# Optimization experiments

Hardware: AMD Instinct MI355X
Metric: run time of the kernel (lower is better)

Reference implementation:

```python
import jax, jax.numpy as jnp
import numpy as np

B, S, D, R, H, NI, NP, NO, K = 2, 2048, 1024, 1024, 8, 8, 32, 8, 3
DH = R // H


def setup_inputs() -> dict:
    key = jax.random.key(0)
    ks = jax.random.split(key, 32)
    rn = lambda k, shp, s=1.0: jax.random.normal(k, shp, jnp.float32) * s
    nrm = lambda v: v / (jnp.linalg.norm(v, axis=-1, keepdims=True) + 1e-8)
    w = 1.0 / np.sqrt(D).astype(np.float32)
    inp = {
        'x': rn(ks[0], (B, S, D)),
        'mask': jnp.tril(jnp.ones((S, S), bool))[None, None],  # causal [1,1,S,S]
        'Wr_in': rn(ks[1], (NI, D), w), 'Wr_proc': rn(ks[2], (NP, D), w), 'Wr_out': rn(ks[3], (NO, D), w),
        'WrO_in': rn(ks[4], (NI, R), w), 'WrO_proc': rn(ks[5], (NP, R), w), 'WrO_out': rn(ks[6], (NO, R), w),
        'Wq_in': rn(ks[7], (NI, D, R), w), 'vq': nrm(rn(ks[8], (NP, R))), 'Wq_out': rn(ks[9], (NO, R, D), w),
        'Wk_in': rn(ks[10], (NI, D, R), w), 'vk': nrm(rn(ks[11], (NP, R))), 'Wk_out': rn(ks[12], (NO, R, D), w),
        'Wv_in': rn(ks[13], (NI, D, R), w), 'vv': nrm(rn(ks[14], (NP, R))), 'Wv_out': rn(ks[15], (NO, R, D), w),
        # circuit_O = NeuronCircuit(rank, d_model): dims swapped
        'Wo_in': rn(ks[16], (NI, R, D), w), 'vo': nrm(rn(ks[17], (NP, D))), 'Wo_out': rn(ks[18], (NO, D, R), w),
    }
    return inp


def _router(x, Wi, Wp, Wo, k):
    in_w = jax.nn.softmax(x @ Wi.T, axis=-1)            # [B,S,NI]
    _, proc_idx = jax.lax.top_k(x @ Wp.T, k)            # [B,S,k]
    out_w = jax.nn.softmax(x @ Wo.T, axis=-1)           # [B,S,NO]
    return in_w, proc_idx, out_w


def _circuit(x, Win, vproc, Wout, in_w, proc_idx, out_w):
    # soft input mix: d_in -> r
    h = jnp.einsum('bsd,ndr,bsn->bsr', x, Win, in_w)
    # k sequential Householder reflections with gathered vectors
    v = vproc[proc_idx]                                 # [B,S,k,r]
    v = v / jnp.sqrt(jnp.sum(v * v, axis=-1, keepdims=True) + 1e-8)
    for i in range(v.shape[2]):
        vi = v[:, :, i, :]
        h = h - 2.0 * vi * jnp.sum(h * vi, axis=-1, keepdims=True)
    # soft output mix: r -> d_out
    return jnp.einsum('bsr,nrd,bsn->bsd', h, Wout, out_w)


def reference(x, mask, Wr_in, Wr_proc, Wr_out, WrO_in, WrO_proc, WrO_out,
              Wq_in, vq, Wq_out, Wk_in, vk, Wk_out, Wv_in, vv, Wv_out,
              Wo_in, vo, Wo_out):
    in_w, pidx, out_w = _router(x, Wr_in, Wr_proc, Wr_out, K)
    Q = _circuit(x, Wq_in, vq, Wq_out, in_w, pidx, out_w)   # [B,S,R]
    Kt = _circuit(x, Wk_in, vk, Wk_out, in_w, pidx, out_w)
    V = _circuit(x, Wv_in, vv, Wv_out, in_w, pidx, out_w)
    q = Q.reshape(B, S, H, DH).transpose(0, 2, 1, 3)
    k = Kt.reshape(B, S, H, DH).transpose(0, 2, 1, 3)
    v = V.reshape(B, S, H, DH).transpose(0, 2, 1, 3)
    scores = jnp.einsum('bhqd,bhkd->bhqk', q, k) / np.sqrt(DH).astype(np.float32)
    scores = jnp.where(mask, scores, jnp.float32(-1e9))
    p = jax.nn.softmax(scores, axis=-1)
    o = jnp.einsum('bhqk,bhkd->bhqd', p, v)
    o = o.transpose(0, 2, 1, 3).reshape(B, S, R)
    in_wO, pidxO, out_wO = _router(o, WrO_in, WrO_proc, WrO_out, K)
    out = _circuit(o, Wo_in, vo, Wo_out, in_wO, pidxO, out_wO)  # [B,S,D]
    return out
```

## Files before the change

### kernel.cpp

```cpp
#include <hip/hip_runtime.h>


typedef __attribute__((ext_vector_type(4))) float f32x4;
typedef _Float16 f16x8 __attribute__((ext_vector_type(8)));
typedef _Float16 f16x4 __attribute__((ext_vector_type(4)));

static constexpr int S_LEN  = 2048;
static constexpr int TOK    = 4096;
static constexpr int DMODEL = 1024;
static constexpr int KDIM   = 8192;

__device__ __forceinline__ void async16(const void* g, void* l) {
  __builtin_amdgcn_global_load_lds(
      (const __attribute__((address_space(1))) void*)g,
      (__attribute__((address_space(3))) void*)l, 16, 0, 0);
}

__global__ __launch_bounds__(256) void split_kernel(const float* __restrict__ X,
                                                    _Float16* __restrict__ Xh,
                                                    _Float16* __restrict__ Xl) {
  size_t i = ((size_t)blockIdx.x * 256 + threadIdx.x) * 4;
  float4 v = *(const float4*)&X[i];
  float a[4] = {v.x, v.y, v.z, v.w};
  f16x4 hv, lv;
#pragma unroll
  for (int e = 0; e < 4; ++e) {
    _Float16 hh = (_Float16)a[e];
    hv[e] = hh;
    lv[e] = (_Float16)(a[e] - (float)hh);
  }
  *(f16x4*)&Xh[i] = hv;
  *(f16x4*)&Xl[i] = lv;
}

__global__ __launch_bounds__(256) void transpose_split(const float* __restrict__ W,
                                                       _Float16* __restrict__ Th,
                                                       _Float16* __restrict__ Tl) {
  __shared__ float tbuf[64][65];
  const int tid = threadIdx.x;
  const int k0 = blockIdx.x * 64, n0 = blockIdx.y * 64;
#pragma unroll
  for (int j = 0; j < 4; ++j) {
    int ci = tid + 256 * j;
    int r = ci >> 4, c4 = (ci & 15) * 4;
    float4 v = *(const float4*)&W[(size_t)(k0 + r) * DMODEL + n0 + c4];
    tbuf[r][c4 + 0] = v.x; tbuf[r][c4 + 1] = v.y;
    tbuf[r][c4 + 2] = v.z; tbuf[r][c4 + 3] = v.w;
  }
  __syncthreads();
#pragma unroll
  for (int j = 0; j < 2; ++j) {
    int ci = tid + 256 * j;
    int nl = ci >> 3, k8 = (ci & 7) * 8;
    f16x8 hv, lv;
#pragma unroll
    for (int e = 0; e < 8; ++e) {
      float v = tbuf[k8 + e][nl];
      _Float16 hh = (_Float16)v;
      hv[e] = hh;
      lv[e] = (_Float16)(v - (float)hh);
    }
    size_t off = (size_t)(n0 + nl) * KDIM + k0 + k8;
    *(f16x8*)&Th[off] = hv;
    *(f16x8*)&Tl[off] = lv;
  }
}

__global__ __launch_bounds__(256) void router_kernel(const float* __restrict__ X,
                                                     const float* __restrict__ Wi,
                                                     const float* __restrict__ Wp,
                                                     const float* __restrict__ Wo,
                                                     float* __restrict__ in_w,
                                                     float* __restrict__ out_w,
                                                     int* __restrict__ pidx) {
  __shared__ float xs[1024];
  __shared__ double lg[48];
  const int t = blockIdx.x, tid = threadIdx.x;
  const int wid = tid >> 6, lane = tid & 63;
#pragma unroll
  for (int j = 0; j < 4; ++j) {
    int d = tid + 256 * j;
    xs[d] = X[(size_t)t * DMODEL + d];
  }
  __syncthreads();
  for (int i = wid; i < 48; i += 4) {
    const float* wrow = (i < 8)  ? Wi + (size_t)i * DMODEL
                      : (i < 40) ? Wp + (size_t)(i - 8) * DMODEL
                                 : Wo + (size_t)(i - 40) * DMODEL;
    double s = 0.0;
#pragma unroll
    for (int j = 0; j < 16; ++j) { int d = lane + 64 * j; s += (double)xs[d] * (double)wrow[d]; }
#pragma unroll
    for (int mm = 32; mm >= 1; mm >>= 1) s += __shfl_xor(s, mm);
    if (lane == 0) lg[i] = s;
  }
  __syncthreads();
  if (tid == 0) {
    float l[8], m;
    for (int i = 0; i < 8; ++i) l[i] = (float)lg[i];
    m = l[0];
    for (int i = 1; i < 8; ++i) m = fmaxf(m, l[i]);
    float e[8], su = 0.f;
    for (int i = 0; i < 8; ++i) { e[i] = expf(l[i] - m); su += e[i]; }
    for (int i = 0; i < 8; ++i) in_w[t * 8 + i] = e[i] / su;
  } else if (tid == 64) {
    float l[8], m;
    for (int i = 0; i < 8; ++i) l[i] = (float)lg[40 + i];
    m = l[0];
    for (int i = 1; i < 8; ++i) m = fmaxf(m, l[i]);
    float e[8], su = 0.f;
    for (int i = 0; i < 8; ++i) { e[i] = expf(l[i] - m); su += e[i]; }
    for (int i = 0; i < 8; ++i) out_w[t * 8 + i] = e[i] / su;
  } else if (tid == 128) {
    unsigned used = 0;
    for (int j = 0; j < 3; ++j) {
      double best = -1e300; int bi = 0;
      for (int i = 0; i < 32; ++i)
        if (!((used >> i) & 1u) && lg[8 + i] > best) { best = lg[8 + i]; bi = i; }
      used |= 1u << bi;
      pidx[t * 3 + j] = bi;
    }
  }
}

__global__ __launch_bounds__(256) void reflect4_kernel(const float* __restrict__ Pa,
                                                       const float* __restrict__ Pb,
                                                       const float* __restrict__ Pc,
                                                       const float* __restrict__ Pd,
                                                       const int* __restrict__ pidx,
                                                       const float* __restrict__ vtab,
                                                       _Float16* __restrict__ Hh,
                                                       _Float16* __restrict__ Hl) {
  __shared__ float red[8];
  const int t = blockIdx.x, tid = threadIdx.x;
  const int wid = tid >> 6, lane = tid & 63;
  size_t gi = (size_t)t * DMODEL + tid * 4;
  float4 ha = *(const float4*)&Pa[gi];
  float4 hb = *(const float4*)&Pb[gi];
  float4 hc = *(const float4*)&Pc[gi];
  float4 hd = *(const float4*)&Pd[gi];
  float4 h = {ha.x + hb.x + hc.x + hd.x, ha.y + hb.y + hc.y + hd.y,
              ha.z + hb.z + hc.z + hd.z, ha.w + hb.w + hc.w + hd.w};
  for (int i = 0; i < 3; ++i) {
    int idx = pidx[t * 3 + i];
    float4 vi = *(const float4*)&vtab[(size_t)idx * DMODEL + tid * 4];
    float hv = h.x * vi.x + h.y * vi.y + h.z * vi.z + h.w * vi.w;
    float vv = vi.x * vi.x + vi.y * vi.y + vi.z * vi.z + vi.w * vi.w;
#pragma unroll
    for (int mm = 32; mm >= 1; mm >>= 1) { hv += __shfl_xor(hv, mm); vv += __shfl_xor(vv, mm); }
    if (lane == 0) { red[wid] = hv; red[4 + wid] = vv; }
    __syncthreads();
    float dot = red[0] + red[1] + red[2] + red[3];
    float vn  = red[4] + red[5] + red[6] + red[7];
    __syncthreads();
    float c = 2.f * dot / (vn + 1e-8f);
    h.x -= c * vi.x; h.y -= c * vi.y; h.z -= c * vi.z; h.w -= c * vi.w;
  }
  float a[4] = {h.x, h.y, h.z, h.w};
  f16x4 hv4, lv4;
#pragma unroll
  for (int e = 0; e < 4; ++e) {
    _Float16 hh = (_Float16)a[e];
    hv4[e] = hh;
    lv4[e] = (_Float16)(a[e] - (float)hh);
  }
  *(f16x4*)&Hh[gi] = hv4;
  *(f16x4*)&Hl[gi] = lv4;
}

__global__ __launch_bounds__(256) void reduce4_planes(const float* __restrict__ a,
                                                      const float* __restrict__ b,
                                                      const float* __restrict__ c,
                                                      const float* __restrict__ d,
                                                      _Float16* __restrict__ Dh,
                                                      _Float16* __restrict__ Dl) {
  size_t i = ((size_t)blockIdx.x * 256 + threadIdx.x) * 4;
  float4 va = *(const float4*)&a[i];
  float4 vb = *(const float4*)&b[i];
  float4 vc = *(const float4*)&c[i];
  float4 vd = *(const float4*)&d[i];
  float s[4] = {va.x + vb.x + vc.x + vd.x, va.y + vb.y + vc.y + vd.y,
                va.z + vb.z + vc.z + vd.z, va.w + vb.w + vc.w + vd.w};
  f16x4 hv, lv;
#pragma unroll
  for (int e = 0; e < 4; ++e) {
    _Float16 hh = (_Float16)s[e];
    hv[e] = hh;
    lv[e] = (_Float16)(s[e] - (float)hh);
  }
  *(f16x4*)&Dh[i] = hv;
  *(f16x4*)&Dl[i] = lv;
}

__global__ __launch_bounds__(256) void reduce4_f32(const float* __restrict__ a,
                                                   const float* __restrict__ b,
                                                   const float* __restrict__ c,
                                                   const float* __restrict__ d,
                                                   float* __restrict__ o) {
  size_t i = ((size_t)blockIdx.x * 256 + threadIdx.x) * 4;
  float4 va = *(const float4*)&a[i];
  float4 vb = *(const float4*)&b[i];
  float4 vc = *(const float4*)&c[i];
  float4 vd = *(const float4*)&d[i];
  float4 vo = {va.x + vb.x + vc.x + vd.x, va.y + vb.y + vc.y + vd.y,
               va.z + vb.z + vc.z + vd.z, va.w + vb.w + vc.w + vd.w};
  *(float4*)&o[i] = vo;
}

template <bool FAST>
__global__ __launch_bounds__(256, 4) void gemm_planes(const _Float16* __restrict__ Ahp,
                                                      const _Float16* __restrict__ Alp,
                                                      const float* __restrict__ wmix,
                                                      const _Float16* __restrict__ Bh,
                                                      const _Float16* __restrict__ Bl,
                                                      float* __restrict__ C0,
                                                      float* __restrict__ C1,
                                                      float* __restrict__ C2,
                                                      float* __restrict__ C3) {
  __shared__ _Float16 sAh[128 * 32], sAl[128 * 32];
  __shared__ _Float16 sBh[128 * 32], sBl[128 * 32];
  __shared__ float sWr[128 * 2];
  const int tid = threadIdx.x;
  const int wid = tid >> 6, lane = tid & 63;
  const int l16 = lane & 15, lhi = lane >> 4;
  const int wr = wid >> 1, wc = wid & 1;
  const int fid = blockIdx.x + (blockIdx.y << 5) + (blockIdx.z << 8);
  const int wg  = ((fid & 7) << 7) + (fid >> 3);
  const int kz  = wg >> 8;
  const int rem = wg & 255;
  const int bm = (rem & 31) * 128;
  const int bn = (rem >> 5) * 128;
  const int kbase = kz * 2048, nb = kz * 2;
  float* __restrict__ Cp = (kz == 0) ? C0 : (kz == 1) ? C1 : (kz == 2) ? C2 : C3;

  {
    int row = tid >> 1, p = tid & 1;
    const float* w = &wmix[(size_t)(bm + row) * 8 + nb];
    sWr[tid] = p ? w[1] : w[0] / w[1];
  }

  f32x4 acc[4][4];
#pragma unroll
  for (int i = 0; i < 4; ++i)
#pragma unroll
    for (int j = 0; j < 4; ++j) { f32x4 z = {0.f, 0.f, 0.f, 0.f}; acc[i][j] = z; }

  for (int kt = 0; kt < 2048; kt += 32) {
    const int kg = kbase + kt, d0 = kg & 1023;
#pragma unroll
    for (int j = 0; j < 2; ++j) {
      int ci = tid + 256 * j;
      int row = ci >> 2, jc = ci & 3;
      int jcs = jc ^ ((row >> 1) & 3);
      size_t ga = (size_t)(bm + row) * DMODEL + d0 + jcs * 8;
      size_t gb = (size_t)(bn + row) * KDIM + kg + jcs * 8;
      async16(&Ahp[ga], &sAh[ci * 8]);
      if (!FAST) async16(&Alp[ga], &sAl[ci * 8]);
      async16(&Bh[gb], &sBh[ci * 8]);
      if (!FAST) async16(&Bl[gb], &sBl[ci * 8]);
    }
    __syncthreads();
    f16x8 fah[4], fal[4], fbh[4], fbl[4];
#pragma unroll
    for (int mi = 0; mi < 4; ++mi) {
      int row = wr * 64 + mi * 16 + l16;
      int idx = row * 32 + ((lhi ^ ((row >> 1) & 3)) * 8);
      fah[mi] = *(const f16x8*)&sAh[idx];
      if (!FAST) fal[mi] = *(const f16x8*)&sAl[idx];
    }
#pragma unroll
    for (int ni = 0; ni < 4; ++ni) {
      int row = wc * 64 + ni * 16 + l16;
      int idx = row * 32 + ((lhi ^ ((row >> 1) & 3)) * 8);
      fbh[ni] = *(const f16x8*)&sBh[idx];
      if (!FAST) fbl[ni] = *(const f16x8*)&sBl[idx];
    }
#pragma unroll
    for (int mi = 0; mi < 4; ++mi)
#pragma unroll
      for (int ni = 0; ni < 4; ++ni) {
        f32x4 a = acc[mi][ni];
        a = __builtin_amdgcn_mfma_f32_16x16x32_f16(fah[mi], fbh[ni], a, 0, 0, 0);
        if (!FAST) {
          a = __builtin_amdgcn_mfma_f32_16x16x32_f16(fah[mi], fbl[ni], a, 0, 0, 0);
          a = __builtin_amdgcn_mfma_f32_16x16x32_f16(fal[mi], fbh[ni], a, 0, 0, 0);
        }
        acc[mi][ni] = a;
      }
    __syncthreads();
    if (kt == 992) {
#pragma unroll
      for (int mi = 0; mi < 4; ++mi)
#pragma unroll
        for (int r = 0; r < 4; ++r) {
          float s = sWr[(wr * 64 + mi * 16 + lhi * 4 + r) * 2];
#pragma unroll
          for (int ni = 0; ni < 4; ++ni) acc[mi][ni][r] *= s;
        }
    }
  }
#pragma unroll
  for (int mi = 0; mi < 4; ++mi)
#pragma unroll
    for (int r = 0; r < 4; ++r) {
      int rowl = wr * 64 + mi * 16 + lhi * 4 + r;
      float s = sWr[rowl * 2 + 1];
#pragma unroll
      for (int ni = 0; ni < 4; ++ni) {
        int col = bn + wc * 64 + ni * 16 + l16;
        Cp[(size_t)(bm + rowl) * DMODEL + col] = acc[mi][ni][r] * s;
      }
    }
}

__global__ __launch_bounds__(256) void vtrans4_kernel(const float* __restrict__ Va,
                                                      const float* __restrict__ Vb,
                                                      const float* __restrict__ Vc,
                                                      const float* __restrict__ Vd,
                                                      _Float16* __restrict__ Vth,
                                                      _Float16* __restrict__ Vtl) {
  __shared__ float tbuf[64][65];
  const int tid = threadIdx.x;
  const int t0 = blockIdx.x * 64, d0 = blockIdx.y * 64, bh = blockIdx.z;
  const int b = bh >> 3, h = bh & 7;
#pragma unroll
  for (int j = 0; j < 4; ++j) {
    int ci = tid + 256 * j;
    int r = ci >> 4, c4 = (ci & 15) * 4;
    size_t g = (size_t)(b * S_LEN + t0 + r) * DMODEL + h * 128 + d0 + c4;
    float4 va = *(const float4*)&Va[g];
    float4 vb = *(const float4*)&Vb[g];
    float4 vc = *(const float4*)&Vc[g];
    float4 vd = *(const float4*)&Vd[g];
    tbuf[r][c4 + 0] = va.x + vb.x + vc.x + vd.x;
    tbuf[r][c4 + 1] = va.y + vb.y + vc.y + vd.y;
    tbuf[r][c4 + 2] = va.z + vb.z + vc.z + vd.z;
    tbuf[r][c4 + 3] = va.w + vb.w + vc.w + vd.w;
  }
  __syncthreads();
#pragma unroll
  for (int j = 0; j < 4; ++j) {
    int ci = tid + 256 * j;
    int r = ci >> 4, c4 = (ci & 15) * 4;
    float s[4] = {tbuf[c4 + 0][r], tbuf[c4 + 1][r], tbuf[c4 + 2][r], tbuf[c4 + 3][r]};
    f16x4 hv, lv;
#pragma unroll
    for (int e = 0; e < 4; ++e) {
      _Float16 hh = (_Float16)s[e];
      hv[e] = hh;
      lv[e] = (_Float16)(s[e] - (float)hh);
    }
    size_t o = ((size_t)bh * 128 + d0 + r) * S_LEN + t0 + c4;
    *(f16x4*)&Vth[o] = hv;
    *(f16x4*)&Vtl[o] = lv;
  }
}

__global__ __launch_bounds__(256) void attn_kernel(const _Float16* __restrict__ Qh,
                                                   const _Float16* __restrict__ Ql,
                                                   const _Float16* __restrict__ Kh,
                                                   const _Float16* __restrict__ Kl,
                                                   const _Float16* __restrict__ Vth,
                                                   const _Float16* __restrict__ Vtl,
                                                   float* __restrict__ O,
                                                   _Float16* __restrict__ Oh) {
  __shared__ _Float16 sKh[32 * 128], sKl[32 * 128];
  __shared__ _Float16 sVh[128 * 32], sVl[128 * 32];
  __shared__ _Float16 sPh[4 * 16 * 32], sPl[4 * 16 * 32];
  const int tid = threadIdx.x;
  const int wid = tid >> 6, lane = tid & 63;
  const int l16 = lane & 15, lhi = lane >> 4;
  const int qt = (gridDim.x - 1) - blockIdx.x;
  const int bh = blockIdx.y;
  const int b = bh >> 3, h = bh & 7;
  const size_t qkbase = (size_t)b * S_LEN * DMODEL + h * 128;
  const float scale = 0.08838834764831845f;

  const int qrow = qt * 64 + wid * 16 + l16;
  const size_t qoff = qkbase + (size_t)qrow * DMODEL;
  f16x8 qh[4], ql[4];
#pragma unroll
  for (int kk = 0; kk < 4; ++kk) {
    qh[kk] = *(const f16x8*)&Qh[qoff + kk * 32 + lhi * 8];
    ql[kk] = *(const f16x8*)&Ql[qoff + kk * 32 + lhi * 8];
  }

  f32x4 of[8];
#pragma unroll
  for (int i = 0; i < 8; ++i) { f32x4 z = {0.f, 0.f, 0.f, 0.f}; of[i] = z; }
  float m_[4], l_[4];
#pragma unroll
  for (int r = 0; r < 4; ++r) { m_[r] = -1e30f; l_[r] = 0.f; }

  const int ntw = qt * 2 + 1 + (wid >> 1);
  const int NT  = qt * 2 + 2;

  for (int kt = 0; kt < NT; ++kt) {
    __syncthreads();
#pragma unroll
    for (int j = 0; j < 2; ++j) {
      int ci = tid + 256 * j;
      int k = ci >> 4, c = ci & 15;
      int cs = c ^ (k & 7);
      size_t g = qkbase + (size_t)(kt * 32 + k) * DMODEL + cs * 8;
      async16(&Kh[g], &sKh[k * 128 + c * 8]);
      async16(&Kl[g], &sKl[k * 128 + c * 8]);
    }
#pragma unroll
    for (int j = 0; j < 2; ++j) {
      int ci = tid + 256 * j;
      int d = ci >> 2, c = ci & 3;
      int cs = c ^ ((d >> 1) & 3);
      size_t g = ((size_t)bh * 128 + d) * S_LEN + kt * 32 + cs * 8;
      async16(&Vth[g], &sVh[d * 32 + c * 8]);
      async16(&Vtl[g], &sVl[d * 32 + c * 8]);
    }
    __syncthreads();

    if (kt < ntw) {
      f32x4 s0 = {0.f, 0.f, 0.f, 0.f}, s1 = {0.f, 0.f, 0.f, 0.f};
#pragma unroll
      for (int kk = 0; kk < 4; ++kk) {
        int col = (kk * 32 + lhi * 8);
        int i0 = l16 * 128 + (col ^ ((l16 & 7) * 8));
        int i1 = (16 + l16) * 128 + (col ^ (((16 + l16) & 7) * 8));
        f16x8 kb0h = *(const f16x8*)&sKh[i0];
        f16x8 kb0l = *(const f16x8*)&sKl[i0];
        f16x8 kb1h = *(const f16x8*)&sKh[i1];
        f16x8 kb1l = *(const f16x8*)&sKl[i1];
        s0 = __builtin_amdgcn_mfma_f32_16x16x32_f16(qh[kk], kb0h, s0, 0, 0, 0);
        s0 = __builtin_amdgcn_mfma_f32_16x16x32_f16(qh[kk], kb0l, s0, 0, 0, 0);
        s0 = __builtin_amdgcn_mfma_f32_16x16x32_f16(ql[kk], kb0h, s0, 0, 0, 0);
        s1 = __builtin_amdgcn_mfma_f32_16x16x32_f16(qh[kk], kb1h, s1, 0, 0, 0);
        s1 = __builtin_amdgcn_mfma_f32_16x16x32_f16(qh[kk], kb1l, s1, 0, 0, 0);
        s1 = __builtin_amdgcn_mfma_f32_16x16x32_f16(ql[kk], kb1h, s1, 0, 0, 0);
      }
      const int qg = qt * 64 + wid * 16 + (lane >> 4) * 4;
      if (kt == ntw - 1) {
#pragma unroll
        for (int r = 0; r < 4; ++r) {
          int q = qg + r;
          int k0 = kt * 32 + l16, k1 = k0 + 16;
          s0[r] = (k0 <= q) ? s0[r] * scale : -1e30f;
          s1[r] = (k1 <= q) ? s1[r] * scale : -1e30f;
        }
      } else {
#pragma unroll
        for (int r = 0; r < 4; ++r) { s0[r] *= scale; s1[r] *= scale; }
      }
      float p0[4], p1[4], fr[4];
#pragma unroll
      for (int r = 0; r < 4; ++r) {
        float rm = fmaxf(s0[r], s1[r]);
        rm = fmaxf(rm, __shfl_xor(rm, 1));
        rm = fmaxf(rm, __shfl_xor(rm, 2));
        rm = fmaxf(rm, __shfl_xor(rm, 4));
        rm = fmaxf(rm, __shfl_xor(rm, 8));
        float mn = fmaxf(m_[r], rm);
        fr[r] = __expf(m_[r] - mn);
        m_[r] = mn;
        p0[r] = __expf(s0[r] - mn);
        p1[r] = __expf(s1[r] - mn);
        float rs = p0[r] + p1[r];
        rs += __shfl_xor(rs, 1);
        rs += __shfl_xor(rs, 2);
        rs += __shfl_xor(rs, 4);
        rs += __shfl_xor(rs, 8);
        l_[r] = l_[r] * fr[r] + rs;
      }
#pragma unroll
      for (int i = 0; i < 8; ++i)
#pragma unroll
        for (int r = 0; r < 4; ++r) of[i][r] *= fr[r];
#pragma unroll
      for (int r = 0; r < 4; ++r) {
        int q = (lane >> 4) * 4 + r;
        int swz = ((q >> 1) & 3) * 8;
        int c0 = l16, c1 = 16 + l16;
        _Float16 h0 = (_Float16)p0[r];
        _Float16 h1 = (_Float16)p1[r];
        sPh[wid * 512 + q * 32 + (c0 ^ swz)] = h0;
        sPl[wid * 512 + q * 32 + (c0 ^ swz)] = (_Float16)(p0[r] - (float)h0);
        sPh[wid * 512 + q * 32 + (c1 ^ swz)] = h1;
        sPl[wid * 512 + q * 32 + (c1 ^ swz)] = (_Float16)(p1[r] - (float)h1);
      }
      int pidxr = wid * 512 + l16 * 32 + ((lhi * 8) ^ (((l16 >> 1) & 3) * 8));
      f16x8 pah = *(const f16x8*)&sPh[pidxr];
      f16x8 pal = *(const f16x8*)&sPl[pidxr];
#pragma unroll
      for (int d16 = 0; d16 < 8; ++d16) {
        int d = d16 * 16 + l16;
        int vidx = d * 32 + ((lhi * 8) ^ (((d >> 1) & 3) * 8));
        f16x8 vbh = *(const f16x8*)&sVh[vidx];
        f16x8 vbl = *(const f16x8*)&sVl[vidx];
        f32x4 a = of[d16];
        a = __builtin_amdgcn_mfma_f32_16x16x32_f16(pah, vbh, a, 0, 0, 0);
        a = __builtin_amdgcn_mfma_f32_16x16x32_f16(pah, vbl, a, 0, 0, 0);
        a = __builtin_amdgcn_mfma_f32_16x16x32_f16(pal, vbh, a, 0, 0, 0);
        of[d16] = a;
      }
    }
  }
  float inv[4];
#pragma unroll
  for (int r = 0; r < 4; ++r) inv[r] = 1.f / l_[r];
  const int qg = qt * 64 + wid * 16 + (lane >> 4) * 4;
#pragma unroll
  for (int d16 = 0; d16 < 8; ++d16)
#pragma unroll
    for (int r = 0; r < 4; ++r) {
      float val = of[d16][r] * inv[r];
      size_t gi = qkbase + (size_t)(qg + r) * DMODEL + d16 * 16 + l16;
      O[gi] = val;
      Oh[gi] = (_Float16)val;
    }
}

extern "C" void kernel_launch(void* const* d_in, const int* in_sizes, int n_in,
                              void* d_out, int out_size, void* d_ws, size_t ws_size,
                              hipStream_t stream) {
  (void)in_sizes; (void)n_in; (void)out_size;
  const float* x        = (const float*)d_in[0];
  const float* Wr_in    = (const float*)d_in[2];
  const float* Wr_proc  = (const float*)d_in[3];
  const float* Wr_out   = (const float*)d_in[4];
  const float* WrO_in   = (const float*)d_in[5];
  const float* WrO_proc = (const float*)d_in[6];
  const float* WrO_out  = (const float*)d_in[7];
  const float* Wq_in    = (const float*)d_in[8];
  const float* vq       = (const float*)d_in[9];
  const float* Wq_out   = (const float*)d_in[10];
  const float* Wk_in    = (const float*)d_in[11];
  const float* vk       = (const float*)d_in[12];
  const float* Wk_out   = (const float*)d_in[13];
  const float* Wv_in    = (const float*)d_in[14];
  const float* vv       = (const float*)d_in[15];
  const float* Wv_out   = (const float*)d_in[16];
  const float* Wo_in    = (const float*)d_in[17];
  const float* vo       = (const float*)d_in[18];
  const float* Wo_out   = (const float*)d_in[19];

  char* wsbase = (char*)d_ws;
  size_t off = 0;
  auto carve = [&](size_t bytes) -> void* {
    void* r = wsbase + off;
    off = (off + bytes + 255) & ~(size_t)255;
    return r;
  };
  const size_t WBYTES = (size_t)KDIM * DMODEL * 2;
  const size_t PBYTES = (size_t)TOK * DMODEL * 2;
  const size_t HBYTES = (size_t)TOK * DMODEL * 4;
  _Float16* WTh = (_Float16*)carve(WBYTES);
  _Float16* WTl = (_Float16*)carve(WBYTES);
  _Float16* Xh  = (_Float16*)carve(PBYTES);
  _Float16* Xl  = (_Float16*)carve(PBYTES);
  _Float16* Hh  = (_Float16*)carve(PBYTES);
  _Float16* Hl  = (_Float16*)carve(PBYTES);
  float* P0 = (float*)carve(HBYTES);
  float* P1 = (float*)carve(HBYTES);
  float* P2 = (float*)carve(HBYTES);
  _Float16* Qph = (_Float16*)carve(PBYTES);
  _Float16* Qpl = (_Float16*)carve(PBYTES);
  _Float16* Kph = (_Float16*)carve(PBYTES);
  _Float16* Kpl = (_Float16*)carve(PBYTES);
  float* iw1 = (float*)carve((size_t)TOK * 8 * 4);
  float* ow1 = (float*)carve((size_t)TOK * 8 * 4);
  float* iw2 = (float*)carve((size_t)TOK * 8 * 4);
  float* ow2 = (float*)carve((size_t)TOK * 8 * 4);
  int* pi1 = (int*)carve((size_t)TOK * 3 * 4);
  int* pi2 = (int*)carve((size_t)TOK * 3 * 4);

  if (off > ws_size) {
    hipMemsetAsync(d_out, 0, (size_t)out_size * 4, stream);
    return;
  }

  float*    Pd  = (float*)d_out;
  float*    PQ  = (float*)Qph;
  float*    PX  = (float*)Xh;
  _Float16* Vth = WTh;
  _Float16* Vtl = WTh + (size_t)TOK * DMODEL;
  float*    Ofp = P0;
  _Float16* Ohp = (_Float16*)P1;

  const dim3 blk(256);
  const dim3 tgrid(KDIM / 64, DMODEL / 64);
  const dim3 ggrid(TOK / 128, DMODEL / 128, 4);
  const dim3 rgrid(TOK * DMODEL / (256 * 4));
  const dim3 vgrid(S_LEN / 64, 2, 16);
  const dim3 agrid(S_LEN / 64, 16);

  split_kernel<<<rgrid, blk, 0, stream>>>(x, Xh, Xl);
  router_kernel<<<TOK, blk, 0, stream>>>(x, Wr_in, Wr_proc, Wr_out, iw1, ow1, pi1);

  transpose_split<<<tgrid, blk, 0, stream>>>(Wq_in, WTh, WTl);
  gemm_planes<false><<<ggrid, blk, 0, stream>>>(Xh, Xl, iw1, WTh, WTl, P0, P1, P2, Pd);
  reflect4_kernel<<<TOK, blk, 0, stream>>>(P0, P1, P2, Pd, pi1, vq, Hh, Hl);
  transpose_split<<<tgrid, blk, 0, stream>>>(Wq_out, WTh, WTl);
  gemm_planes<false><<<ggrid, blk, 0, stream>>>(Hh, Hl, ow1, WTh, WTl, P0, P1, P2, Pd);
  reduce4_planes<<<rgrid, blk, 0, stream>>>(P0, P1, P2, Pd, Qph, Qpl);

  transpose_split<<<tgrid, blk, 0, stream>>>(Wk_in, WTh, WTl);
  gemm_planes<false><<<ggrid, blk, 0, stream>>>(Xh, Xl, iw1, WTh, WTl, P0, P1, P2, Pd);
  reflect4_kernel<<<TOK, blk, 0, stream>>>(P0, P1, P2, Pd, pi1, vk, Hh, Hl);
  transpose_split<<<tgrid, blk, 0, stream>>>(Wk_out, WTh, WTl);
  gemm_planes<false><<<ggrid, blk, 0, stream>>>(Hh, Hl, ow1, WTh, WTl, P0, P1, P2, Pd);
  reduce4_planes<<<rgrid, blk, 0, stream>>>(P0, P1, P2, Pd, Kph, Kpl);

  transpose_split<<<tgrid, blk, 0, stream>>>(Wv_in, WTh, WTl);
  gemm_planes<false><<<ggrid, blk, 0, stream>>>(Xh, Xl, iw1, WTh, WTl, P0, P1, P2, Pd);
  reflect4_kernel<<<TOK, blk, 0, stream>>>(P0, P1, P2, Pd, pi1, vv, Hh, Hl);
  transpose_split<<<tgrid, blk, 0, stream>>>(Wv_out, WTh, WTl);
  gemm_planes<false><<<ggrid, blk, 0, stream>>>(Hh, Hl, ow1, WTh, WTl, P0, P1, P2, Pd);
  vtrans4_kernel<<<vgrid, blk, 0, stream>>>(P0, P1, P2, Pd, Vth, Vtl);

  attn_kernel<<<agrid, blk, 0, stream>>>(Qph, Qpl, Kph, Kpl, Vth, Vtl, Ofp, Ohp);

  router_kernel<<<TOK, blk, 0, stream>>>(Ofp, WrO_in, WrO_proc, WrO_out, iw2, ow2, pi2);
  transpose_split<<<tgrid, blk, 0, stream>>>(Wo_in, WTh, WTl);
  gemm_planes<true><<<ggrid, blk, 0, stream>>>(Ohp, Ohp, iw2, WTh, WTl, PX, P0, P2, Pd);
  reflect4_kernel<<<TOK, blk, 0, stream>>>(PX, P0, P2, Pd, pi2, vo, Hh, Hl);
  transpose_split<<<tgrid, blk, 0, stream>>>(Wo_out, WTh, WTl);
  gemm_planes<true><<<ggrid, blk, 0, stream>>>(Hh, Hh, ow2, WTh, WTl, P0, P1, P2, PQ);
  reduce4_f32<<<rgrid, blk, 0, stream>>>(P0, P1, P2, PQ, (float*)d_out);
}
```

Before: 1.834 ms.

## Switch GEMM to 32x32x16 MFMA with pre-swizzled LDS layout, fuse split into router

The planes GEMM now uses 32x32x16 MFMA instructions with a 2x2 accumulator tile per wave instead of 4x4 16x16x32 tiles. Shared memory is laid out in fragment order, which removes the XOR swizzle on reads. The FAST path uses a deeper K step of 64 and shrinks the unused low-plane buffers. The separate fp16 hi/lo split kernel is folded into the first router kernel, saving one launch and one read of x. The goal is fewer LDS reads per MFMA and less launch and memory traffic, at the cost of possible bank conflicts in the new unswizzled layout.

```diff
diff --git a/kernel.cpp b/kernel.cpp
--- a/kernel.cpp
+++ b/kernel.cpp
@@ -1,7 +1,8 @@
 #include <hip/hip_runtime.h>
 
 
-typedef __attribute__((ext_vector_type(4))) float f32x4;
+typedef __attribute__((ext_vector_type(4)))  float f32x4;
+typedef __attribute__((ext_vector_type(16))) float f32x16;
 typedef _Float16 f16x8 __attribute__((ext_vector_type(8)));
 typedef _Float16 f16x4 __attribute__((ext_vector_type(4)));
 
@@ -14,23 +15,6 @@
   __builtin_amdgcn_global_load_lds(
       (const __attribute__((address_space(1))) void*)g,
       (__attribute__((address_space(3))) void*)l, 16, 0, 0);
-}
-
-__global__ __launch_bounds__(256) void split_kernel(const float* __restrict__ X,
-                                                    _Float16* __restrict__ Xh,
-                                                    _Float16* __restrict__ Xl) {
-  size_t i = ((size_t)blockIdx.x * 256 + threadIdx.x) * 4;
-  float4 v = *(const float4*)&X[i];
-  float a[4] = {v.x, v.y, v.z, v.w};
-  f16x4 hv, lv;
-#pragma unroll
-  for (int e = 0; e < 4; ++e) {
-    _Float16 hh = (_Float16)a[e];
-    hv[e] = hh;
-    lv[e] = (_Float16)(a[e] - (float)hh);
-  }
-  *(f16x4*)&Xh[i] = hv;
-  *(f16x4*)&Xl[i] = lv;
 }
 
 __global__ __launch_bounds__(256) void transpose_split(const float* __restrict__ W,
@@ -72,7 +56,9 @@
                                                      const float* __restrict__ Wo,
                                                      float* __restrict__ in_w,
                                                      float* __restrict__ out_w,
-                                                     int* __restrict__ pidx) {
+                                                     int* __restrict__ pidx,
+                                                     _Float16* __restrict__ Xh,
+                                                     _Float16* __restrict__ Xl) {
   __shared__ float xs[1024];
   __shared__ double lg[48];
   const int t = blockIdx.x, tid = threadIdx.x;
@@ -121,6 +107,16 @@
       pidx[t * 3 + j] = bi;
     }
   }
+  if (Xh != nullptr) {
+#pragma unroll
+    for (int j = 0; j < 4; ++j) {
+      int d = tid + 256 * j;
+      float v = xs[d];
+      _Float16 hh = (_Float16)v;
+      Xh[(size_t)t * DMODEL + d] = hh;
+      Xl[(size_t)t * DMODEL + d] = (_Float16)(v - (float)hh);
+    }
+  }
 }
 
 __global__ __launch_bounds__(256) void reflect4_kernel(const float* __restrict__ Pa,
@@ -217,13 +213,18 @@
                                                       float* __restrict__ C1,
                                                       float* __restrict__ C2,
                                                       float* __restrict__ C3) {
-  __shared__ _Float16 sAh[128 * 32], sAl[128 * 32];
-  __shared__ _Float16 sBh[128 * 32], sBl[128 * 32];
+  constexpr int BK  = FAST ? 64 : 32;
+  constexpr int NKS = BK / 16;
+  constexpr int CHUNKS = 128 * BK / 8;
+  __shared__ _Float16 sAh[128 * BK];
+  __shared__ _Float16 sBh[128 * BK];
+  __shared__ _Float16 sAl[FAST ? 8 : 128 * BK];
+  __shared__ _Float16 sBl[FAST ? 8 : 128 * BK];
   __shared__ float sWr[128 * 2];
   const int tid = threadIdx.x;
   const int wid = tid >> 6, lane = tid & 63;
-  const int l16 = lane & 15, lhi = lane >> 4;
   const int wr = wid >> 1, wc = wid & 1;
+  const int l31 = lane & 31, l5 = lane >> 5;
   const int fid = blockIdx.x + (blockIdx.y << 5) + (blockIdx.z << 8);
   const int wg  = ((fid & 7) << 7) + (fid >> 3);
   const int kz  = wg >> 8;
@@ -239,75 +240,84 @@
     sWr[tid] = p ? w[1] : w[0] / w[1];
   }
 
-  f32x4 acc[4][4];
-#pragma unroll
-  for (int i = 0; i < 4; ++i)
-#pragma unroll
-    for (int j = 0; j < 4; ++j) { f32x4 z = {0.f, 0.f, 0.f, 0.f}; acc[i][j] = z; }
-
-  for (int kt = 0; kt < 2048; kt += 32) {
+  f32x16 acc[2][2];
+#pragma unroll
+  for (int i = 0; i < 2; ++i)
+#pragma unroll
+    for (int j = 0; j < 2; ++j)
+#pragma unroll
+      for (int r = 0; r < 16; ++r) acc[i][j][r] = 0.f;
+
+  for (int kt = 0; kt < 2048; kt += BK) {
     const int kg = kbase + kt, d0 = kg & 1023;
 #pragma unroll
-    for (int j = 0; j < 2; ++j) {
-      int ci = tid + 256 * j;
-      int row = ci >> 2, jc = ci & 3;
-      int jcs = jc ^ ((row >> 1) & 3);
-      size_t ga = (size_t)(bm + row) * DMODEL + d0 + jcs * 8;
-      size_t gb = (size_t)(bn + row) * KDIM + kg + jcs * 8;
-      async16(&Ahp[ga], &sAh[ci * 8]);
-      if (!FAST) async16(&Alp[ga], &sAl[ci * 8]);
-      async16(&Bh[gb], &sBh[ci * 8]);
-      if (!FAST) async16(&Bl[gb], &sBl[ci * 8]);
+    for (int j = 0; j < CHUNKS / 256; ++j) {
+      int q = tid + 256 * j;
+      int rb = q >> (FAST ? 8 : 7);
+      int kk = (q >> 6) & (NKS - 1);
+      int l  = q & 63;
+      int rowoff = rb * 32 + (l & 31);
+      int koff   = kk * 16 + (l >> 5) * 8;
+      size_t ga = (size_t)(bm + rowoff) * DMODEL + d0 + koff;
+      size_t gb = (size_t)(bn + rowoff) * KDIM  + kg + koff;
+      async16(&Ahp[ga], &sAh[q * 8]);
+      async16(&Bh[gb],  &sBh[q * 8]);
+      if (!FAST) {
+        async16(&Alp[ga], &sAl[q * 8]);
+        async16(&Bl[gb],  &sBl[q * 8]);
+      }
     }
     __syncthreads();
-    f16x8 fah[4], fal[4], fbh[4], fbl[4];
-#pragma unroll
-    for (int mi = 0; mi < 4; ++mi) {
-      int row = wr * 64 + mi * 16 + l16;
-      int idx = row * 32 + ((lhi ^ ((row >> 1) & 3)) * 8);
-      fah[mi] = *(const f16x8*)&sAh[idx];
-      if (!FAST) fal[mi] = *(const f16x8*)&sAl[idx];
-    }
-#pragma unroll
-    for (int ni = 0; ni < 4; ++ni) {
-      int row = wc * 64 + ni * 16 + l16;
-      int idx = row * 32 + ((lhi ^ ((row >> 1) & 3)) * 8);
-      fbh[ni] = *(const f16x8*)&sBh[idx];
-      if (!FAST) fbl[ni] = *(const f16x8*)&sBl[idx];
-    }
-#pragma unroll
-    for (int mi = 0; mi < 4; ++mi)
-#pragma unroll
-      for (int ni = 0; ni < 4; ++ni) {
-        f32x4 a = acc[mi][ni];
-        a = __builtin_amdgcn_mfma_f32_16x16x32_f16(fah[mi], fbh[ni], a, 0, 0, 0);
-        if (!FAST) {
-          a = __builtin_amdgcn_mfma_f32_16x16x32_f16(fah[mi], fbl[ni], a, 0, 0, 0);
-          a = __builtin_amdgcn_mfma_f32_16x16x32_f16(fal[mi], fbh[ni], a, 0, 0, 0);
+#pragma unroll
+    for (int kk = 0; kk < NKS; ++kk) {
+      f16x8 a_h[2], b_h[2], a_l[2], b_l[2];
+#pragma unroll
+      for (int mi = 0; mi < 2; ++mi) {
+        int qa = (((wr * 2 + mi) * NKS + kk) * 64 + lane) * 8;
+        a_h[mi] = *(const f16x8*)&sAh[qa];
+        if (!FAST) a_l[mi] = *(const f16x8*)&sAl[qa];
+      }
+#pragma unroll
+      for (int ni = 0; ni < 2; ++ni) {
+        int qb = (((wc * 2 + ni) * NKS + kk) * 64 + lane) * 8;
+        b_h[ni] = *(const f16x8*)&sBh[qb];
+        if (!FAST) b_l[ni] = *(const f16x8*)&sBl[qb];
+      }
+#pragma unroll
+      for (int mi = 0; mi < 2; ++mi)
+#pragma unroll
+        for (int ni = 0; ni < 2; ++ni) {
+          f32x16 a = acc[mi][ni];
+          a = __builtin_amdgcn_mfma_f32_32x32x16_f16(a_h[mi], b_h[ni], a, 0, 0, 0);
+          if (!FAST) {
+            a = __builtin_amdgcn_mfma_f32_32x32x16_f16(a_h[mi], b_l[ni], a, 0, 0, 0);
+            a = __builtin_amdgcn_mfma_f32_32x32x16_f16(a_l[mi], b_h[ni], a, 0, 0, 0);
+          }
+          acc[mi][ni] = a;
         }
-        acc[mi][ni] = a;
-      }
+    }
     __syncthreads();
-    if (kt == 992) {
-#pragma unroll
-      for (int mi = 0; mi < 4; ++mi)
-#pragma unroll
-        for (int r = 0; r < 4; ++r) {
-          float s = sWr[(wr * 64 + mi * 16 + lhi * 4 + r) * 2];
-#pragma unroll
-          for (int ni = 0; ni < 4; ++ni) acc[mi][ni][r] *= s;
+    if (kt == 1024 - BK) {
+#pragma unroll
+      for (int mi = 0; mi < 2; ++mi)
+#pragma unroll
+        for (int r = 0; r < 16; ++r) {
+          int rowl = wr * 64 + mi * 32 + (r & 3) + 8 * (r >> 2) + 4 * l5;
+          float s = sWr[rowl * 2];
+#pragma unroll
+          for (int ni = 0; ni < 2; ++ni) acc[mi][ni][r] *= s;
         }
     }
   }
 #pragma unroll
-  for (int mi = 0; mi < 4; ++mi)
-#pragma unroll
-    for (int r = 0; r < 4; ++r) {
-      int rowl = wr * 64 + mi * 16 + lhi * 4 + r;
+  for (int mi = 0; mi < 2; ++mi)
+#pragma unroll
+    for (int r = 0; r < 16; ++r) {
+      int rowl = wr * 64 + mi * 32 + (r & 3) + 8 * (r >> 2) + 4 * l5;
       float s = sWr[rowl * 2 + 1];
 #pragma unroll
-      for (int ni = 0; ni < 4; ++ni) {
-        int col = bn + wc * 64 + ni * 16 + l16;
+      for (int ni = 0; ni < 2; ++ni) {
+        int col = bn + wc * 64 + ni * 32 + l31;
         Cp[(size_t)(bm + rowl) * DMODEL + col] = acc[mi][ni][r] * s;
       }
     }
@@ -590,8 +600,7 @@
   const dim3 vgrid(S_LEN / 64, 2, 16);
   const dim3 agrid(S_LEN / 64, 16);
 
-  split_kernel<<<rgrid, blk, 0, stream>>>(x, Xh, Xl);
-  router_kernel<<<TOK, blk, 0, stream>>>(x, Wr_in, Wr_proc, Wr_out, iw1, ow1, pi1);
+  router_kernel<<<TOK, blk, 0, stream>>>(x, Wr_in, Wr_proc, Wr_out, iw1, ow1, pi1, Xh, Xl);
 
   transpose_split<<<tgrid, blk, 0, stream>>>(Wq_in, WTh, WTl);
   gemm_planes<false><<<ggrid, blk, 0, stream>>>(Xh, Xl, iw1, WTh, WTl, P0, P1, P2, Pd);
@@ -616,7 +625,8 @@
 
   attn_kernel<<<agrid, blk, 0, stream>>>(Qph, Qpl, Kph, Kpl, Vth, Vtl, Ofp, Ohp);
 
-  router_kernel<<<TOK, blk, 0, stream>>>(Ofp, WrO_in, WrO_proc, WrO_out, iw2, ow2, pi2);
+  router_kernel<<<TOK, blk, 0, stream>>>(Ofp, WrO_in, WrO_proc, WrO_out, iw2, ow2, pi2,
+                                         nullptr, nullptr);
   transpose_split<<<tgrid, blk, 0, stream>>>(Wo_in, WTh, WTl);
   gemm_planes<true><<<ggrid, blk, 0, stream>>>(Ohp, Ohp, iw2, WTh, WTl, PX, P0, P2, Pd);
   reflect4_kernel<<<TOK, blk, 0, stream>>>(PX, P0, P2, Pd, pi2, vo, Hh, Hl);
```

Measured after the change: 2.319 ms. +26.5%, slower.

## Enlarge GEMM tiles to 256x256 with 512 threads; fuse fp16 split into router

Applied to the files above, without the earlier changes.

The split-K fp16-plane GEMM now uses 256x256 output tiles with 8 waves per block, each wave holding an 8x4 grid of MFMA accumulators. This raises data reuse per LDS load and halves the number of blocks. In FAST mode the low-plane LDS buffers are shrunk. Separately, the input hi/lo fp16 split moves into the router kernel, which already holds x in shared memory, so one launch and one pass over x are removed. The larger tiles mean more registers and fewer blocks (256 per GEMM), which lowers occupancy and may leave compute units idle.

```diff
diff --git a/kernel.cpp b/kernel.cpp
--- a/kernel.cpp
+++ b/kernel.cpp
@@ -14,23 +14,6 @@
   __builtin_amdgcn_global_load_lds(
       (const __attribute__((address_space(1))) void*)g,
       (__attribute__((address_space(3))) void*)l, 16, 0, 0);
-}
-
-__global__ __launch_bounds__(256) void split_kernel(const float* __restrict__ X,
-                                                    _Float16* __restrict__ Xh,
-                                                    _Float16* __restrict__ Xl) {
-  size_t i = ((size_t)blockIdx.x * 256 + threadIdx.x) * 4;
-  float4 v = *(const float4*)&X[i];
-  float a[4] = {v.x, v.y, v.z, v.w};
-  f16x4 hv, lv;
-#pragma unroll
-  for (int e = 0; e < 4; ++e) {
-    _Float16 hh = (_Float16)a[e];
-    hv[e] = hh;
-    lv[e] = (_Float16)(a[e] - (float)hh);
-  }
-  *(f16x4*)&Xh[i] = hv;
-  *(f16x4*)&Xl[i] = lv;
 }
 
 __global__ __launch_bounds__(256) void transpose_split(const float* __restrict__ W,
@@ -72,7 +55,9 @@
                                                      const float* __restrict__ Wo,
                                                      float* __restrict__ in_w,
                                                      float* __restrict__ out_w,
-                                                     int* __restrict__ pidx) {
+                                                     int* __restrict__ pidx,
+                                                     _Float16* __restrict__ Xh,
+                                                     _Float16* __restrict__ Xl) {
   __shared__ float xs[1024];
   __shared__ double lg[48];
   const int t = blockIdx.x, tid = threadIdx.x;
@@ -121,6 +106,16 @@
       pidx[t * 3 + j] = bi;
     }
   }
+  if (Xh != nullptr) {
+#pragma unroll
+    for (int j = 0; j < 4; ++j) {
+      int d = tid + 256 * j;
+      float v = xs[d];
+      _Float16 hh = (_Float16)v;
+      Xh[(size_t)t * DMODEL + d] = hh;
+      Xl[(size_t)t * DMODEL + d] = (_Float16)(v - (float)hh);
+    }
+  }
 }
 
 __global__ __launch_bounds__(256) void reflect4_kernel(const float* __restrict__ Pa,
@@ -208,7 +203,7 @@
 }
 
 template <bool FAST>
-__global__ __launch_bounds__(256, 4) void gemm_planes(const _Float16* __restrict__ Ahp,
+__global__ __launch_bounds__(512, 2) void gemm_planes(const _Float16* __restrict__ Ahp,
                                                       const _Float16* __restrict__ Alp,
                                                       const float* __restrict__ wmix,
                                                       const _Float16* __restrict__ Bh,
@@ -217,19 +212,20 @@
                                                       float* __restrict__ C1,
                                                       float* __restrict__ C2,
                                                       float* __restrict__ C3) {
-  __shared__ _Float16 sAh[128 * 32], sAl[128 * 32];
-  __shared__ _Float16 sBh[128 * 32], sBl[128 * 32];
-  __shared__ float sWr[128 * 2];
+  __shared__ _Float16 sAh[256 * 32];
+  __shared__ _Float16 sBh[256 * 32];
+  __shared__ _Float16 sAl[FAST ? 8 : 256 * 32];
+  __shared__ _Float16 sBl[FAST ? 8 : 256 * 32];
+  __shared__ float sWr[256 * 2];
   const int tid = threadIdx.x;
   const int wid = tid >> 6, lane = tid & 63;
   const int l16 = lane & 15, lhi = lane >> 4;
-  const int wr = wid >> 1, wc = wid & 1;
-  const int fid = blockIdx.x + (blockIdx.y << 5) + (blockIdx.z << 8);
-  const int wg  = ((fid & 7) << 7) + (fid >> 3);
-  const int kz  = wg >> 8;
-  const int rem = wg & 255;
-  const int bm = (rem & 31) * 128;
-  const int bn = (rem >> 5) * 128;
+  const int wr = wid >> 2, wc = wid & 3;
+  const int fid = blockIdx.x + (blockIdx.y << 4) + (blockIdx.z << 6);
+  const int wg  = ((fid & 7) << 5) + (fid >> 3);
+  const int bm = (wg & 15) * 256;
+  const int bn = ((wg >> 4) & 3) * 256;
+  const int kz = wg >> 6;
   const int kbase = kz * 2048, nb = kz * 2;
   float* __restrict__ Cp = (kz == 0) ? C0 : (kz == 1) ? C1 : (kz == 2) ? C2 : C3;
 
@@ -239,9 +235,9 @@
     sWr[tid] = p ? w[1] : w[0] / w[1];
   }
 
-  f32x4 acc[4][4];
-#pragma unroll
-  for (int i = 0; i < 4; ++i)
+  f32x4 acc[8][4];
+#pragma unroll
+  for (int i = 0; i < 8; ++i)
 #pragma unroll
     for (int j = 0; j < 4; ++j) { f32x4 z = {0.f, 0.f, 0.f, 0.f}; acc[i][j] = z; }
 
@@ -249,61 +245,62 @@
     const int kg = kbase + kt, d0 = kg & 1023;
 #pragma unroll
     for (int j = 0; j < 2; ++j) {
-      int ci = tid + 256 * j;
+      int ci = tid + 512 * j;
       int row = ci >> 2, jc = ci & 3;
       int jcs = jc ^ ((row >> 1) & 3);
       size_t ga = (size_t)(bm + row) * DMODEL + d0 + jcs * 8;
       size_t gb = (size_t)(bn + row) * KDIM + kg + jcs * 8;
       async16(&Ahp[ga], &sAh[ci * 8]);
-      if (!FAST) async16(&Alp[ga], &sAl[ci * 8]);
-      async16(&Bh[gb], &sBh[ci * 8]);
-      if (!FAST) async16(&Bl[gb], &sBl[ci * 8]);
+      async16(&Bh[gb],  &sBh[ci * 8]);
+      if (!FAST) {
+        async16(&Alp[ga], &sAl[ci * 8]);
+        async16(&Bl[gb],  &sBl[ci * 8]);
+      }
     }
     __syncthreads();
-    f16x8 fah[4], fal[4], fbh[4], fbl[4];
-#pragma unroll
-    for (int mi = 0; mi < 4; ++mi) {
-      int row = wr * 64 + mi * 16 + l16;
-      int idx = row * 32 + ((lhi ^ ((row >> 1) & 3)) * 8);
-      fah[mi] = *(const f16x8*)&sAh[idx];
-      if (!FAST) fal[mi] = *(const f16x8*)&sAl[idx];
-    }
+    f16x8 b_h[4], b_l[4];
 #pragma unroll
     for (int ni = 0; ni < 4; ++ni) {
       int row = wc * 64 + ni * 16 + l16;
       int idx = row * 32 + ((lhi ^ ((row >> 1) & 3)) * 8);
-      fbh[ni] = *(const f16x8*)&sBh[idx];
-      if (!FAST) fbl[ni] = *(const f16x8*)&sBl[idx];
-    }
-#pragma unroll
-    for (int mi = 0; mi < 4; ++mi)
+      b_h[ni] = *(const f16x8*)&sBh[idx];
+      if (!FAST) b_l[ni] = *(const f16x8*)&sBl[idx];
+    }
+#pragma unroll
+    for (int mi = 0; mi < 8; ++mi) {
+      int rowa = wr * 128 + mi * 16 + l16;
+      int idxa = rowa * 32 + ((lhi ^ ((rowa >> 1) & 3)) * 8);
+      f16x8 a_h = *(const f16x8*)&sAh[idxa];
+      f16x8 a_l;
+      if (!FAST) a_l = *(const f16x8*)&sAl[idxa];
 #pragma unroll
       for (int ni = 0; ni < 4; ++ni) {
         f32x4 a = acc[mi][ni];
-        a = __builtin_amdgcn_mfma_f32_16x16x32_f16(fah[mi], fbh[ni], a, 0, 0, 0);
+        a = __builtin_amdgcn_mfma_f32_16x16x32_f16(a_h, b_h[ni], a, 0, 0, 0);
         if (!FAST) {
-          a = __builtin_amdgcn_mfma_f32_16x16x32_f16(fah[mi], fbl[ni], a, 0, 0, 0);
-          a = __builtin_amdgcn_mfma_f32_16x16x32_f16(fal[mi], fbh[ni], a, 0, 0, 0);
+          a = __builtin_amdgcn_mfma_f32_16x16x32_f16(a_h, b_l[ni], a, 0, 0, 0);
+          a = __builtin_amdgcn_mfma_f32_16x16x32_f16(a_l, b_h[ni], a, 0, 0, 0);
         }
         acc[mi][ni] = a;
       }
+    }
     __syncthreads();
     if (kt == 992) {
 #pragma unroll
-      for (int mi = 0; mi < 4; ++mi)
+      for (int mi = 0; mi < 8; ++mi)
 #pragma unroll
         for (int r = 0; r < 4; ++r) {
-          float s = sWr[(wr * 64 + mi * 16 + lhi * 4 + r) * 2];
+          float s = sWr[(wr * 128 + mi * 16 + lhi * 4 + r) * 2];
 #pragma unroll
           for (int ni = 0; ni < 4; ++ni) acc[mi][ni][r] *= s;
         }
     }
   }
 #pragma unroll
-  for (int mi = 0; mi < 4; ++mi)
+  for (int mi = 0; mi < 8; ++mi)
 #pragma unroll
     for (int r = 0; r < 4; ++r) {
-      int rowl = wr * 64 + mi * 16 + lhi * 4 + r;
+      int rowl = wr * 128 + mi * 16 + lhi * 4 + r;
       float s = sWr[rowl * 2 + 1];
 #pragma unroll
       for (int ni = 0; ni < 4; ++ni) {
@@ -584,43 +581,44 @@
   _Float16* Ohp = (_Float16*)P1;
 
   const dim3 blk(256);
+  const dim3 gblk(512);
   const dim3 tgrid(KDIM / 64, DMODEL / 64);
-  const dim3 ggrid(TOK / 128, DMODEL / 128, 4);
+  const dim3 ggrid(TOK / 256, DMODEL / 256, 4);
   const dim3 rgrid(TOK * DMODEL / (256 * 4));
   const dim3 vgrid(S_LEN / 64, 2, 16);
   const dim3 agrid(S_LEN / 64, 16);
 
-  split_kernel<<<rgrid, blk, 0, stream>>>(x, Xh, Xl);
-  router_kernel<<<TOK, blk, 0, stream>>>(x, Wr_in, Wr_proc, Wr_out, iw1, ow1, pi1);
+  router_kernel<<<TOK, blk, 0, stream>>>(x, Wr_in, Wr_proc, Wr_out, iw1, ow1, pi1, Xh, Xl);
 
   transpose_split<<<tgrid, blk, 0, stream>>>(Wq_in, WTh, WTl);
-  gemm_planes<false><<<ggrid, blk, 0, stream>>>(Xh, Xl, iw1, WTh, WTl, P0, P1, P2, Pd);
+  gemm_planes<false><<<ggrid, gblk, 0, stream>>>(Xh, Xl, iw1, WTh, WTl, P0, P1, P2, Pd);
   reflect4_kernel<<<TOK, blk, 0, stream>>>(P0, P1, P2, Pd, pi1, vq, Hh, Hl);
   transpose_split<<<tgrid, blk, 0, stream>>>(Wq_out, WTh, WTl);
-  gemm_planes<false><<<ggrid, blk, 0, stream>>>(Hh, Hl, ow1, WTh, WTl, P0, P1, P2, Pd);
+  gemm_planes<false><<<ggrid, gblk, 0, stream>>>(Hh, Hl, ow1, WTh, WTl, P0, P1, P2, Pd);
   reduce4_planes<<<rgrid, blk, 0, stream>>>(P0, P1, P2, Pd, Qph, Qpl);
 
   transpose_split<<<tgrid, blk, 0, stream>>>(Wk_in, WTh, WTl);
-  gemm_planes<false><<<ggrid, blk, 0, stream>>>(Xh, Xl, iw1, WTh, WTl, P0, P1, P2, Pd);
+  gemm_planes<false><<<ggrid, gblk, 0, stream>>>(Xh, Xl, iw1, WTh, WTl, P0, P1, P2, Pd);
   reflect4_kernel<<<TOK, blk, 0, stream>>>(P0, P1, P2, Pd, pi1, vk, Hh, Hl);
   transpose_split<<<tgrid, blk, 0, stream>>>(Wk_out, WTh, WTl);
-  gemm_planes<false><<<ggrid, blk, 0, stream>>>(Hh, Hl, ow1, WTh, WTl, P0, P1, P2, Pd);
+  gemm_planes<false><<<ggrid, gblk, 0, stream>>>(Hh, Hl, ow1, WTh, WTl, P0, P1, P2, Pd);
   reduce4_planes<<<rgrid, blk, 0, stream>>>(P0, P1, P2, Pd, Kph, Kpl);
 
   transpose_split<<<tgrid, blk, 0, stream>>>(Wv_in, WTh, WTl);
-  gemm_planes<false><<<ggrid, blk, 0, stream>>>(Xh, Xl, iw1, WTh, WTl, P0, P1, P2, Pd);
+  gemm_planes<false><<<ggrid, gblk, 0, stream>>>(Xh, Xl, iw1, WTh, WTl, P0, P1, P2, Pd);
   reflect4_kernel<<<TOK, blk, 0, stream>>>(P0, P1, P2, Pd, pi1, vv, Hh, Hl);
   transpose_split<<<tgrid, blk, 0, stream>>>(Wv_out, WTh, WTl);
-  gemm_planes<false><<<ggrid, blk, 0, stream>>>(Hh, Hl, ow1, WTh, WTl, P0, P1, P2, Pd);
+  gemm_planes<false><<<ggrid, gblk, 0, stream>>>(Hh, Hl, ow1, WTh, WTl, P0, P1, P2, Pd);
   vtrans4_kernel<<<vgrid, blk, 0, stream>>>(P0, P1, P2, Pd, Vth, Vtl);
 
   attn_kernel<<<agrid, blk, 0, stream>>>(Qph, Qpl, Kph, Kpl, Vth, Vtl, Ofp, Ohp);
 
-  router_kernel<<<TOK, blk, 0, stream>>>(Ofp, WrO_in, WrO_proc, WrO_out, iw2, ow2, pi2);
+  router_kernel<<<TOK, blk, 0, stream>>>(Ofp, WrO_in, WrO_proc, WrO_out, iw2, ow2, pi2,
+                                         nullptr, nullptr);
   transpose_split<<<tgrid, blk, 0, stream>>>(Wo_in, WTh, WTl);
-  gemm_planes<true><<<ggrid, blk, 0, stream>>>(Ohp, Ohp, iw2, WTh, WTl, PX, P0, P2, Pd);
+  gemm_planes<true><<<ggrid, gblk, 0, stream>>>(Ohp, Ohp, iw2, WTh, WTl, PX, P0, P2, Pd);
   reflect4_kernel<<<TOK, blk, 0, stream>>>(PX, P0, P2, Pd, pi2, vo, Hh, Hl);
   transpose_split<<<tgrid, blk, 0, stream>>>(Wo_out, WTh, WTl);
-  gemm_planes<true><<<ggrid, blk, 0, stream>>>(Hh, Hh, ow2, WTh, WTl, P0, P1, P2, PQ);
+  gemm_planes<true><<<ggrid, gblk, 0, stream>>>(Hh, Hh, ow2, WTh, WTl, P0, P1, P2, PQ);
   reduce4_f32<<<rgrid, blk, 0, stream>>>(P0, P1, P2, PQ, (float*)d_out);
 }
```

Measured after the change: 1.747 ms. 1.05x faster.
